# Kernel tuning notes

Hardware: AMD Instinct MI355X
Metric: run time of the kernel (lower is better)

Reference implementation:

```python
import jax, jax.numpy as jnp
import numpy as np

V, E = 50000, 800000
NODE_IN, EDGE_IN, OUT, HEADS = 128, 16, 32, 4
NEG_SLOPE = 0.2  # DGL EdgeGATConv default negative_slope


def setup_inputs() -> dict:
    key = jax.random.key(0)
    ks = jax.random.split(key, 10)
    return {
        "node_feats": jax.random.normal(ks[0], (V, NODE_IN), jnp.float32),
        "edge_feats": jax.random.normal(ks[1], (E, EDGE_IN), jnp.float32),
        "src": jax.random.randint(ks[2], (E,), 0, V),
        "dst": jax.random.randint(ks[3], (E,), 0, V),
        "W_node": jax.random.normal(ks[4], (NODE_IN, HEADS * OUT), jnp.float32) * 0.05,
        "W_edge": jax.random.normal(ks[5], (EDGE_IN, HEADS * OUT), jnp.float32) * 0.05,
        "attn_l": jax.random.normal(ks[6], (HEADS, OUT), jnp.float32) * 0.05,
        "attn_r": jax.random.normal(ks[7], (HEADS, OUT), jnp.float32) * 0.05,
        "attn_e": jax.random.normal(ks[8], (HEADS, OUT), jnp.float32) * 0.05,
        "res_W": jax.random.normal(ks[9], (NODE_IN, HEADS * OUT), jnp.float32) * 0.05,
        "bias": jnp.zeros((HEADS * OUT,), jnp.float32),
    }


def _leaky_relu(x, slope):
    return jnp.where(x >= 0, x, slope * x)


def reference(node_feats, edge_feats, src, dst, W_node, W_edge, attn_l, attn_r, attn_e, res_W, bias):
    V = node_feats.shape[0]
    H, F = attn_l.shape
    # linear projections
    ft = (node_feats @ W_node).reshape(V, H, F)    # [V,H,F]
    fe = (edge_feats @ W_edge).reshape(-1, H, F)   # [E,H,F]
    # per-head attention logits
    el = jnp.einsum('vhf,hf->vh', ft, attn_l)      # [V,H]
    er = jnp.einsum('vhf,hf->vh', ft, attn_r)      # [V,H]
    ee = jnp.einsum('ehf,hf->eh', fe, attn_e)      # [E,H]
    e = _leaky_relu(el[src] + er[dst] + ee, NEG_SLOPE)  # [E,H]
    # edge softmax over incoming edges of each destination node (stable)
    emax = jax.ops.segment_max(e, dst, num_segments=V)  # [V,H]
    ex = jnp.exp(e - emax[dst])
    esum = jax.ops.segment_sum(ex, dst, num_segments=V)  # [V,H]
    a = ex / esum[dst]                                   # [E,H]
    # weighted message passing: u_mul_e(ft, a) then sum to dst
    msg = ft[src] * a[:, :, None]                        # [E,H,F]
    rst = jax.ops.segment_sum(msg, dst, num_segments=V)  # [V,H,F]
    # residual connection + bias (EdgeGATConv residual=True, bias=True)
    rst = rst + (node_feats @ res_W).reshape(V, H, F)
    rst = rst + bias.reshape(1, H, F)
    # agg_mode='flatten': concat heads
    return rst.reshape(V, H * F)
```

## Files before the change

kernel.cpp:

```cpp
#include <hip/hip_runtime.h>
#include <hip/hip_fp16.h>
#include <cstdint>

#define V_N 50000
#define E_N 800000
#define NODE_IN 128
#define EDGE_IN 16
#define HF 128
#define NEG_SLOPE 0.2f
#define NB_SCAN 196

#define OFF_FT    0
#define OFF_EL    3200000
#define OFF_ER    3400000
#define OFF_DEG   3600000
#define OFF_ROW   3650000
#define OFF_BSUM  3700004
#define OFF_RANK  3700260
#define OFF_REC   4500260
#define OFF_WATT  7700260
#define OFF_BFRAG 7700324

typedef short bf16x8 __attribute__((ext_vector_type(8)));
typedef float f32x4 __attribute__((ext_vector_type(4)));

__device__ __forceinline__ unsigned short f2bf(float f) {
    unsigned u = __float_as_uint(f);
    u += 0x7fffu + ((u >> 16) & 1u);
    return (unsigned short)(u >> 16);
}
__device__ __forceinline__ unsigned pk2(float lo, float hi) {
    return (unsigned)f2bf(lo) | ((unsigned)f2bf(hi) << 16);
}
__device__ __forceinline__ float bflo(unsigned w) { return __uint_as_float(w << 16); }
__device__ __forceinline__ float bfhi(unsigned w) { return __uint_as_float(w & 0xffff0000u); }

typedef __fp16 fp16x2 __attribute__((ext_vector_type(2)));
__device__ __forceinline__ unsigned pkh2(float a, float b) {
    fp16x2 h = __builtin_amdgcn_cvt_pkrtz(a, b);
    return __builtin_bit_cast(unsigned, h);
}
__device__ __forceinline__ __half2 u2h(unsigned u) {
    return __builtin_bit_cast(__half2, u);
}
__device__ __forceinline__ unsigned h2u(__half2 h) {
    return __builtin_bit_cast(unsigned, h);
}

__global__ void k_prep(const float* __restrict__ We,
                       const float* __restrict__ attn_e,
                       const float* __restrict__ Wn,
                       const float* __restrict__ Wr,
                       float* __restrict__ watt,
                       unsigned* __restrict__ bfrag,
                       int* __restrict__ deg) {
    int g = blockIdx.x * 256 + threadIdx.x;
    for (int i = g; i < V_N; i += 16384) deg[i] = 0;
    if (blockIdx.x == 0 && threadIdx.x < 64) {
        int k = threadIdx.x >> 2, h = threadIdx.x & 3;
        float s = 0.f;
        #pragma unroll
        for (int f = 0; f < 32; f++)
            s += We[k * HF + h * 32 + f] * attn_e[h * 32 + f];
        watt[k * 4 + h] = s;
    }
    if (g < 16384) {
        int c    = g >> 8;
        int lane = (g >> 2) & 63;
        int jp   = g & 3;
        int nt = c >> 2, ks = c & 3;
        int col = nt * 16 + (lane & 15);
        int k   = ks * 32 + (lane >> 4) * 8 + jp * 2;
        const float* W = (col < 128) ? Wn : Wr;
        int cc = col & 127;
        float x0 = W[(size_t)k * 128 + cc];
        float x1 = W[(size_t)(k + 1) * 128 + cc];
        bfrag[g] = pk2(x0, x1);
    }
}

__global__ __launch_bounds__(256) void k_node(
    const float* __restrict__ nf, const unsigned* __restrict__ bfragw,
    const float* __restrict__ attn_l, const float* __restrict__ attn_r,
    const float* __restrict__ bias,
    unsigned* __restrict__ ftw, float* __restrict__ el,
    float* __restrict__ er, float* __restrict__ out)
{
    __shared__ __align__(16) float sSf[32 * 140];
    unsigned short* sA = (unsigned short*)sSf;

    const int t = threadIdx.x;
    const int lane = t & 63;
    const int w = t >> 6;
    const int nb = blockIdx.x * 32;
    const int n15 = lane & 15;
    const int q = lane >> 4;
    const unsigned short* bfrag = (const unsigned short*)bfragw;

    #pragma unroll
    for (int i = 0; i < 4; i++) {
        int f = t + i * 256;
        int node = f >> 5;
        int kc = (f & 31) * 4;
        float4 v = {0.f, 0.f, 0.f, 0.f};
        if (nb + node < V_N)
            v = *(const float4*)(nf + (size_t)(nb + node) * NODE_IN + kc);
        uint2 u2 = make_uint2(pk2(v.x, v.y), pk2(v.z, v.w));
        *(uint2*)&sA[node * 136 + kc] = u2;
    }
    __syncthreads();

    f32x4 acc[2][4];
    #pragma unroll
    for (int m = 0; m < 2; m++)
        #pragma unroll
        for (int tt = 0; tt < 4; tt++) acc[m][tt] = (f32x4){0.f, 0.f, 0.f, 0.f};

    #pragma unroll
    for (int ks = 0; ks < 4; ks++) {
        bf16x8 a0 = *(const bf16x8*)&sA[n15 * 136 + ks * 32 + q * 8];
        bf16x8 a1 = *(const bf16x8*)&sA[(16 + n15) * 136 + ks * 32 + q * 8];
        #pragma unroll
        for (int tt = 0; tt < 4; tt++) {
            int nt = (tt < 2) ? (2 * w + tt) : (8 + 2 * w + (tt - 2));
            bf16x8 b = *(const bf16x8*)(bfrag + ((size_t)(nt * 4 + ks) * 64 + lane) * 8);
            acc[0][tt] = __builtin_amdgcn_mfma_f32_16x16x32_bf16(a0, b, acc[0][tt], 0, 0, 0);
            acc[1][tt] = __builtin_amdgcn_mfma_f32_16x16x32_bf16(a1, b, acc[1][tt], 0, 0, 0);
        }
    }

    {
        float al0 = attn_l[w * 32 + n15];
        float al1 = attn_l[w * 32 + 16 + n15];
        float ar0 = attn_r[w * 32 + n15];
        float ar1 = attn_r[w * 32 + 16 + n15];
        #pragma unroll
        for (int m = 0; m < 2; m++) {
            #pragma unroll
            for (int r = 0; r < 4; r++) {
                float fa = acc[m][0][r], fb = acc[m][1][r];
                float elp = fa * al0 + fb * al1;
                float erp = fa * ar0 + fb * ar1;
                elp += __shfl_xor(elp, 1); erp += __shfl_xor(erp, 1);
                elp += __shfl_xor(elp, 2); erp += __shfl_xor(erp, 2);
                elp += __shfl_xor(elp, 4); erp += __shfl_xor(erp, 4);
                elp += __shfl_xor(elp, 8); erp += __shfl_xor(erp, 8);
                int node = nb + m * 16 + q * 4 + r;
                if (n15 == 0 && node < V_N) {
                    el[node * 4 + w] = elp;
                    er[node * 4 + w] = erp;
                }
            }
        }
    }
    #pragma unroll
    for (int m = 0; m < 2; m++)
        #pragma unroll
        for (int r = 0; r < 4; r++) {
            int node = nb + m * 16 + q * 4 + r;
            if (node < V_N)
                ftw[(size_t)node * 64 + w * 16 + n15] =
                    pkh2(acc[m][0][r], acc[m][1][r]);
        }
    __syncthreads();

    #pragma unroll
    for (int m = 0; m < 2; m++)
        #pragma unroll
        for (int tt = 2; tt < 4; tt++)
            #pragma unroll
            for (int r = 0; r < 4; r++)
                sSf[(m * 16 + q * 4 + r) * 140 + w * 32 + (tt - 2) * 16 + n15] =
                    acc[m][tt][r];
    __syncthreads();
    #pragma unroll
    for (int i = 0; i < 4; i++) {
        int u = t + i * 256;
        int node = u >> 5, c4 = (u & 31) * 4;
        if (nb + node < V_N) {
            float4 v = *(float4*)&sSf[node * 140 + c4];
            float4 b4 = *(const float4*)(bias + c4);
            v.x += b4.x; v.y += b4.y; v.z += b4.z; v.w += b4.w;
            *(float4*)(out + (size_t)(nb + node) * HF + c4) = v;
        }
    }
}

__global__ void k_hist(const int* __restrict__ dst, int* __restrict__ deg,
                       int* __restrict__ rank) {
    int e = blockIdx.x * 256 + threadIdx.x;
    if (e < E_N) rank[e] = atomicAdd(&deg[dst[e]], 1);
}

__global__ __launch_bounds__(256) void k_scan1(const int* __restrict__ deg,
                                               int* __restrict__ rowp,
                                               int* __restrict__ bsum) {
    __shared__ int sh[256];
    int t = threadIdx.x, b = blockIdx.x;
    int i = b * 256 + t;
    int v = (i < V_N) ? deg[i] : 0;
    sh[t] = v;
    __syncthreads();
    #pragma unroll
    for (int off = 1; off < 256; off <<= 1) {
        int u = (t >= off) ? sh[t - off] : 0;
        __syncthreads();
        sh[t] += u;
        __syncthreads();
    }
    if (i < V_N) rowp[i] = sh[t] - v;
    if (t == 255) bsum[b] = sh[255];
}

__global__ __launch_bounds__(256) void k_scan23(int* __restrict__ rowp,
                                                const int* __restrict__ bsum) {
    __shared__ int sh[256];
    int t = threadIdx.x, b = blockIdx.x;
    int v = (t < NB_SCAN) ? bsum[t] : 0;
    sh[t] = v;
    __syncthreads();
    #pragma unroll
    for (int off = 1; off < 256; off <<= 1) {
        int u = (t >= off) ? sh[t - off] : 0;
        __syncthreads();
        sh[t] += u;
        __syncthreads();
    }
    int boff = (b == 0) ? 0 : sh[b - 1];
    int i = b * 256 + t;
    if (i < V_N) rowp[i] += boff;
    if (i == 0) rowp[V_N] = E_N;
}

__global__ __launch_bounds__(256) void k_escatter(
    const float* __restrict__ ef, const int* __restrict__ src,
    const int* __restrict__ dst, const int* __restrict__ rank,
    const int* __restrict__ rowp, const float* __restrict__ watt,
    const float* __restrict__ el, uint4* __restrict__ rec)
{
    __shared__ float sw[64];
    __shared__ __align__(16) float see[256][4];
    const int t = threadIdx.x;
    if (t < 64) sw[t] = watt[t];
    __syncthreads();
    const int base = blockIdx.x * 256;
    const int lane = t & 63, w = t >> 6;
    const int k0 = (lane & 3) * 4;

    #pragma unroll
    for (int r = 0; r < 4; r++) {
        int le = w * 64 + r * 16 + (lane >> 2);
        float4 v = *(const float4*)(ef + (size_t)(base + le) * EDGE_IN + k0);
        float e0 = 0.f, e1 = 0.f, e2 = 0.f, e3 = 0.f;
        float vv[4] = {v.x, v.y, v.z, v.w};
        #pragma unroll
        for (int j = 0; j < 4; j++) {
            int k = k0 + j;
            e0 += vv[j] * sw[k * 4 + 0];
            e1 += vv[j] * sw[k * 4 + 1];
            e2 += vv[j] * sw[k * 4 + 2];
            e3 += vv[j] * sw[k * 4 + 3];
        }
        e0 += __shfl_xor(e0, 1); e1 += __shfl_xor(e1, 1);
        e2 += __shfl_xor(e2, 1); e3 += __shfl_xor(e3, 1);
        e0 += __shfl_xor(e0, 2); e1 += __shfl_xor(e1, 2);
        e2 += __shfl_xor(e2, 2); e3 += __shfl_xor(e3, 2);
        if ((lane & 3) == 0) {
            float4 o = {e0, e1, e2, e3};
            *(float4*)&see[le][0] = o;
        }
    }
    __syncthreads();

    int e = base + t;
    int s = src[e], d = dst[e];
    int p = rowp[d] + rank[e];
    float4 ee = *(float4*)&see[t][0];
    float4 el4 = *(const float4*)(el + (size_t)s * 4);
    uint4 rr;
    rr.x = (unsigned)s;
    rr.y = pk2(el4.x + ee.x, el4.y + ee.y);
    rr.z = pk2(el4.z + ee.z, el4.w + ee.w);
    rr.w = 0;
    rec[p] = rr;
}

__global__ __launch_bounds__(256) void k_gather(
    const int* __restrict__ row, const uint4* __restrict__ rec,
    const float* __restrict__ er,
    const unsigned* __restrict__ ftw, float* __restrict__ out)
{
    __shared__ unsigned aw[4][64][4];
    const int lane = threadIdx.x & 63;
    const int wid  = threadIdx.x >> 6;
    const int d = blockIdx.x * 4 + wid;
    if (d >= V_N) return;
    const int n0 = row[d];
    const int deg = row[d + 1] - n0;
    if (deg == 0) return;

    const float4 er4 = *(const float4*)(er + (size_t)d * 4);

    const int qw = lane >> 4, li = lane & 15;
    const int head = li >> 2;
    float4 s4 = {0.f, 0.f, 0.f, 0.f};
    __half2 ha0 = u2h(0u), ha1 = u2h(0u), ha2 = u2h(0u), ha3 = u2h(0u);
    __half2 hb0 = u2h(0u), hb1 = u2h(0u), hb2 = u2h(0u), hb3 = u2h(0u);

    for (int i0 = 0; i0 < deg; i0 += 64) {
        int chunk = min(64, deg - i0);
        int si = 0;
        float4 ex = {0.f, 0.f, 0.f, 0.f};
        if (lane < chunk) {
            uint4 r = rec[n0 + i0 + lane];
            si = (int)r.x;
            float x0 = bflo(r.y) + er4.x;
            float x1 = bfhi(r.y) + er4.y;
            float x2 = bflo(r.z) + er4.z;
            float x3 = bfhi(r.z) + er4.w;
            x0 = x0 >= 0.f ? x0 : NEG_SLOPE * x0;
            x1 = x1 >= 0.f ? x1 : NEG_SLOPE * x1;
            x2 = x2 >= 0.f ? x2 : NEG_SLOPE * x2;
            x3 = x3 >= 0.f ? x3 : NEG_SLOPE * x3;
            ex.x = __expf(x0); ex.y = __expf(x1);
            ex.z = __expf(x2); ex.w = __expf(x3);
            s4.x += ex.x; s4.y += ex.y; s4.z += ex.z; s4.w += ex.w;
        }
        uint4 ap;
        ap.x = pkh2(ex.x, ex.x); ap.y = pkh2(ex.y, ex.y);
        ap.z = pkh2(ex.z, ex.z); ap.w = pkh2(ex.w, ex.w);
        *(uint4*)&aw[wid][lane][0] = ap;
        asm volatile("s_waitcnt lgkmcnt(0)" ::: "memory");

        int iters = (chunk + 7) & ~7;
        for (int j = 0; j < iters; j += 8) {
            int jq0 = j + qw, jq1 = j + qw + 4;
            int sidx0 = __shfl(si, jq0);
            int sidx1 = __shfl(si, jq1);
            unsigned au0 = aw[wid][jq0][head];
            unsigned au1 = aw[wid][jq1][head];
            uint4 wv0 = *(const uint4*)(ftw + (size_t)sidx0 * 64 + li * 4);
            uint4 wv1 = *(const uint4*)(ftw + (size_t)sidx1 * 64 + li * 4);
            ha0 = __hfma2(u2h(wv0.x), u2h(au0), ha0);
            ha1 = __hfma2(u2h(wv0.y), u2h(au0), ha1);
            ha2 = __hfma2(u2h(wv0.z), u2h(au0), ha2);
            ha3 = __hfma2(u2h(wv0.w), u2h(au0), ha3);
            hb0 = __hfma2(u2h(wv1.x), u2h(au1), hb0);
            hb1 = __hfma2(u2h(wv1.y), u2h(au1), hb1);
            hb2 = __hfma2(u2h(wv1.z), u2h(au1), hb2);
            hb3 = __hfma2(u2h(wv1.w), u2h(au1), hb3);
        }
    }
    #pragma unroll
    for (int off = 1; off < 64; off <<= 1) {
        s4.x += __shfl_xor(s4.x, off);
        s4.y += __shfl_xor(s4.y, off);
        s4.z += __shfl_xor(s4.z, off);
        s4.w += __shfl_xor(s4.w, off);
    }
    ha0 = __hadd2(ha0, hb0); ha1 = __hadd2(ha1, hb1);
    ha2 = __hadd2(ha2, hb2); ha3 = __hadd2(ha3, hb3);
    ha0 = __hadd2(ha0, u2h(__shfl_xor(h2u(ha0), 16)));
    ha1 = __hadd2(ha1, u2h(__shfl_xor(h2u(ha1), 16)));
    ha2 = __hadd2(ha2, u2h(__shfl_xor(h2u(ha2), 16)));
    ha3 = __hadd2(ha3, u2h(__shfl_xor(h2u(ha3), 16)));
    ha0 = __hadd2(ha0, u2h(__shfl_xor(h2u(ha0), 32)));
    ha1 = __hadd2(ha1, u2h(__shfl_xor(h2u(ha1), 32)));
    ha2 = __hadd2(ha2, u2h(__shfl_xor(h2u(ha2), 32)));
    ha3 = __hadd2(ha3, u2h(__shfl_xor(h2u(ha3), 32)));
    if (qw == 0) {
        float rsv = 1.f / (head == 0 ? s4.x : head == 1 ? s4.y :
                           head == 2 ? s4.z : s4.w);
        float* op = out + (size_t)d * HF + head * 32 + (li & 3) * 4;
        float4 r0 = *(float4*)op;
        r0.x += __low2float(ha0) * rsv; r0.y += __low2float(ha1) * rsv;
        r0.z += __low2float(ha2) * rsv; r0.w += __low2float(ha3) * rsv;
        *(float4*)op = r0;
        float4 r1 = *(float4*)(op + 16);
        r1.x += __high2float(ha0) * rsv; r1.y += __high2float(ha1) * rsv;
        r1.z += __high2float(ha2) * rsv; r1.w += __high2float(ha3) * rsv;
        *(float4*)(op + 16) = r1;
    }
}

extern "C" void kernel_launch(void* const* d_in, const int* in_sizes, int n_in,
                              void* d_out, int out_size, void* d_ws, size_t ws_size,
                              hipStream_t stream) {
    const float* nf     = (const float*)d_in[0];
    const float* ef     = (const float*)d_in[1];
    const int*   src    = (const int*)d_in[2];
    const int*   dst    = (const int*)d_in[3];
    const float* Wn     = (const float*)d_in[4];
    const float* We     = (const float*)d_in[5];
    const float* attn_l = (const float*)d_in[6];
    const float* attn_r = (const float*)d_in[7];
    const float* attn_e = (const float*)d_in[8];
    const float* Wr     = (const float*)d_in[9];
    const float* bias   = (const float*)d_in[10];
    float* out = (float*)d_out;

    unsigned* wsw  = (unsigned*)d_ws;
    unsigned* ftw  = wsw + OFF_FT;
    float* el      = (float*)(wsw + OFF_EL);
    float* er      = (float*)(wsw + OFF_ER);
    int* deg       = (int*)(wsw + OFF_DEG);
    int* rowp      = (int*)(wsw + OFF_ROW);
    int* bsum      = (int*)(wsw + OFF_BSUM);
    int* rank      = (int*)(wsw + OFF_RANK);
    uint4* rec     = (uint4*)(wsw + OFF_REC);
    float* watt    = (float*)(wsw + OFF_WATT);
    unsigned* bfrag = wsw + OFF_BFRAG;

    k_prep<<<64, 256, 0, stream>>>(We, attn_e, Wn, Wr, watt, bfrag, deg);
    k_hist<<<(E_N + 255) / 256, 256, 0, stream>>>(dst, deg, rank);
    k_scan1<<<NB_SCAN, 256, 0, stream>>>(deg, rowp, bsum);
    k_scan23<<<NB_SCAN, 256, 0, stream>>>(rowp, bsum);
    k_node<<<(V_N + 31) / 32, 256, 0, stream>>>(nf, bfrag, attn_l, attn_r,
                                                bias, ftw, el, er, out);
    k_escatter<<<E_N / 256, 256, 0, stream>>>(ef, src, dst, rank,
                                              rowp, watt, el, rec);
    k_gather<<<(V_N + 3) / 4, 256, 0, stream>>>(rowp, rec, er, ftw, out);
}
```

Baseline: 243.1 us.

## Fuse prep, histogram, node GEMM and scan into one cooperative kernel

Merges the five setup kernels (weight prep, degree histogram, node projection GEMM, two-level scan) into a single cooperative kernel of 512 persistent blocks, with grid.sync between the dependent phases. The histogram and the node GEMM now run in the same phase and can overlap. The aim is to remove several kernel launch gaps and tail effects. In exchange it adds grid-wide barriers, uses a smaller grid for the GEMM and histogram work, and requires all 512 blocks to be co-resident.

```diff
diff --git a/kernel.cpp b/kernel.cpp
--- a/kernel.cpp
+++ b/kernel.cpp
@@ -1,6 +1,9 @@
 #include <hip/hip_runtime.h>
 #include <hip/hip_fp16.h>
+#include <hip/hip_cooperative_groups.h>
 #include <cstdint>
+
+namespace cg = cooperative_groups;
 
 #define V_N 50000
 #define E_N 800000
@@ -9,6 +12,7 @@
 #define HF 128
 #define NEG_SLOPE 0.2f
 #define NB_SCAN 196
+#define COOP_GRID 512
 
 #define OFF_FT    0
 #define OFF_EL    3200000
@@ -47,17 +51,33 @@
     return __builtin_bit_cast(unsigned, h);
 }
 
-__global__ void k_prep(const float* __restrict__ We,
-                       const float* __restrict__ attn_e,
-                       const float* __restrict__ Wn,
-                       const float* __restrict__ Wr,
-                       float* __restrict__ watt,
-                       unsigned* __restrict__ bfrag,
-                       int* __restrict__ deg) {
-    int g = blockIdx.x * 256 + threadIdx.x;
-    for (int i = g; i < V_N; i += 16384) deg[i] = 0;
-    if (blockIdx.x == 0 && threadIdx.x < 64) {
-        int k = threadIdx.x >> 2, h = threadIdx.x & 3;
+__global__ __launch_bounds__(256, 2) void k_setup(
+    const float* __restrict__ nf,
+    const float* __restrict__ We, const float* __restrict__ attn_e,
+    const float* __restrict__ Wn, const float* __restrict__ Wr,
+    const float* __restrict__ attn_l, const float* __restrict__ attn_r,
+    const float* __restrict__ bias,
+    const int* __restrict__ dst,
+    float* __restrict__ watt, unsigned* __restrict__ bfragw,
+    int* __restrict__ deg, int* __restrict__ rank,
+    int* __restrict__ rowp, int* __restrict__ bsum,
+    unsigned* __restrict__ ftw, float* __restrict__ el,
+    float* __restrict__ er, float* __restrict__ out)
+{
+    cg::grid_group grid = cg::this_grid();
+
+    __shared__ __align__(16) float sSf[32 * 140];
+    unsigned short* sA = (unsigned short*)sSf;
+    int* sh = (int*)sSf;
+
+    const int t = threadIdx.x;
+    const int b = blockIdx.x;
+    const int g = b * 256 + t;
+    const int GSZ = COOP_GRID * 256;
+
+    if (g < V_N) deg[g] = 0;
+    if (b == 0 && t < 64) {
+        int k = t >> 2, h = t & 3;
         float s = 0.f;
         #pragma unroll
         for (int f = 0; f < 32; f++)
@@ -75,161 +95,146 @@
         int cc = col & 127;
         float x0 = W[(size_t)k * 128 + cc];
         float x1 = W[(size_t)(k + 1) * 128 + cc];
-        bfrag[g] = pk2(x0, x1);
-    }
-}
-
-__global__ __launch_bounds__(256) void k_node(
-    const float* __restrict__ nf, const unsigned* __restrict__ bfragw,
-    const float* __restrict__ attn_l, const float* __restrict__ attn_r,
-    const float* __restrict__ bias,
-    unsigned* __restrict__ ftw, float* __restrict__ el,
-    float* __restrict__ er, float* __restrict__ out)
-{
-    __shared__ __align__(16) float sSf[32 * 140];
-    unsigned short* sA = (unsigned short*)sSf;
-
-    const int t = threadIdx.x;
-    const int lane = t & 63;
-    const int w = t >> 6;
-    const int nb = blockIdx.x * 32;
-    const int n15 = lane & 15;
-    const int q = lane >> 4;
-    const unsigned short* bfrag = (const unsigned short*)bfragw;
-
-    #pragma unroll
-    for (int i = 0; i < 4; i++) {
-        int f = t + i * 256;
-        int node = f >> 5;
-        int kc = (f & 31) * 4;
-        float4 v = {0.f, 0.f, 0.f, 0.f};
-        if (nb + node < V_N)
-            v = *(const float4*)(nf + (size_t)(nb + node) * NODE_IN + kc);
-        uint2 u2 = make_uint2(pk2(v.x, v.y), pk2(v.z, v.w));
-        *(uint2*)&sA[node * 136 + kc] = u2;
-    }
-    __syncthreads();
-
-    f32x4 acc[2][4];
-    #pragma unroll
-    for (int m = 0; m < 2; m++)
-        #pragma unroll
-        for (int tt = 0; tt < 4; tt++) acc[m][tt] = (f32x4){0.f, 0.f, 0.f, 0.f};
-
-    #pragma unroll
-    for (int ks = 0; ks < 4; ks++) {
-        bf16x8 a0 = *(const bf16x8*)&sA[n15 * 136 + ks * 32 + q * 8];
-        bf16x8 a1 = *(const bf16x8*)&sA[(16 + n15) * 136 + ks * 32 + q * 8];
-        #pragma unroll
-        for (int tt = 0; tt < 4; tt++) {
-            int nt = (tt < 2) ? (2 * w + tt) : (8 + 2 * w + (tt - 2));
-            bf16x8 b = *(const bf16x8*)(bfrag + ((size_t)(nt * 4 + ks) * 64 + lane) * 8);
-            acc[0][tt] = __builtin_amdgcn_mfma_f32_16x16x32_bf16(a0, b, acc[0][tt], 0, 0, 0);
-            acc[1][tt] = __builtin_amdgcn_mfma_f32_16x16x32_bf16(a1, b, acc[1][tt], 0, 0, 0);
-        }
-    }
+        bfragw[g] = pk2(x0, x1);
+    }
+    grid.sync();
+
+    for (int e = g; e < E_N; e += GSZ)
+        rank[e] = atomicAdd(&deg[dst[e]], 1);
 
     {
-        float al0 = attn_l[w * 32 + n15];
-        float al1 = attn_l[w * 32 + 16 + n15];
-        float ar0 = attn_r[w * 32 + n15];
-        float ar1 = attn_r[w * 32 + 16 + n15];
-        #pragma unroll
-        for (int m = 0; m < 2; m++) {
-            #pragma unroll
-            for (int r = 0; r < 4; r++) {
-                float fa = acc[m][0][r], fb = acc[m][1][r];
-                float elp = fa * al0 + fb * al1;
-                float erp = fa * ar0 + fb * ar1;
-                elp += __shfl_xor(elp, 1); erp += __shfl_xor(erp, 1);
-                elp += __shfl_xor(elp, 2); erp += __shfl_xor(erp, 2);
-                elp += __shfl_xor(elp, 4); erp += __shfl_xor(erp, 4);
-                elp += __shfl_xor(elp, 8); erp += __shfl_xor(erp, 8);
-                int node = nb + m * 16 + q * 4 + r;
-                if (n15 == 0 && node < V_N) {
-                    el[node * 4 + w] = elp;
-                    er[node * 4 + w] = erp;
+        const int lane = t & 63;
+        const int w = t >> 6;
+        const int n15 = lane & 15;
+        const int q = lane >> 4;
+        const unsigned short* bfrag = (const unsigned short*)bfragw;
+        const float al0 = attn_l[w * 32 + n15];
+        const float al1 = attn_l[w * 32 + 16 + n15];
+        const float ar0 = attn_r[w * 32 + n15];
+        const float ar1 = attn_r[w * 32 + 16 + n15];
+
+        for (int tile = b; tile < (V_N + 31) / 32; tile += COOP_GRID) {
+            const int nb = tile * 32;
+            __syncthreads();
+
+            #pragma unroll
+            for (int i = 0; i < 4; i++) {
+                int f = t + i * 256;
+                int node = f >> 5;
+                int kc = (f & 31) * 4;
+                float4 v = {0.f, 0.f, 0.f, 0.f};
+                if (nb + node < V_N)
+                    v = *(const float4*)(nf + (size_t)(nb + node) * NODE_IN + kc);
+                uint2 u2 = make_uint2(pk2(v.x, v.y), pk2(v.z, v.w));
+                *(uint2*)&sA[node * 136 + kc] = u2;
+            }
+            __syncthreads();
+
+            f32x4 acc[2][4];
+            #pragma unroll
+            for (int m = 0; m < 2; m++)
+                #pragma unroll
+                for (int tt = 0; tt < 4; tt++) acc[m][tt] = (f32x4){0.f, 0.f, 0.f, 0.f};
+
+            #pragma unroll
+            for (int ks = 0; ks < 4; ks++) {
+                bf16x8 a0 = *(const bf16x8*)&sA[n15 * 136 + ks * 32 + q * 8];
+                bf16x8 a1 = *(const bf16x8*)&sA[(16 + n15) * 136 + ks * 32 + q * 8];
+                #pragma unroll
+                for (int tt = 0; tt < 4; tt++) {
+                    int nt = (tt < 2) ? (2 * w + tt) : (8 + 2 * w + (tt - 2));
+                    bf16x8 bv = *(const bf16x8*)(bfrag + ((size_t)(nt * 4 + ks) * 64 + lane) * 8);
+                    acc[0][tt] = __builtin_amdgcn_mfma_f32_16x16x32_bf16(a0, bv, acc[0][tt], 0, 0, 0);
+                    acc[1][tt] = __builtin_amdgcn_mfma_f32_16x16x32_bf16(a1, bv, acc[1][tt], 0, 0, 0);
                 }
             }
-        }
-    }
-    #pragma unroll
-    for (int m = 0; m < 2; m++)
+
+            #pragma unroll
+            for (int m = 0; m < 2; m++) {
+                #pragma unroll
+                for (int r = 0; r < 4; r++) {
+                    float fa = acc[m][0][r], fb = acc[m][1][r];
+                    float elp = fa * al0 + fb * al1;
+                    float erp = fa * ar0 + fb * ar1;
+                    elp += __shfl_xor(elp, 1); erp += __shfl_xor(erp, 1);
+                    elp += __shfl_xor(elp, 2); erp += __shfl_xor(erp, 2);
+                    elp += __shfl_xor(elp, 4); erp += __shfl_xor(erp, 4);
+                    elp += __shfl_xor(elp, 8); erp += __shfl_xor(erp, 8);
+                    int node = nb + m * 16 + q * 4 + r;
+                    if (n15 == 0 && node < V_N) {
+                        el[node * 4 + w] = elp;
+                        er[node * 4 + w] = erp;
+                    }
+                }
+            }
+            #pragma unroll
+            for (int m = 0; m < 2; m++)
+                #pragma unroll
+                for (int r = 0; r < 4; r++) {
+                    int node = nb + m * 16 + q * 4 + r;
+                    if (node < V_N)
+                        ftw[(size_t)node * 64 + w * 16 + n15] =
+                            pkh2(acc[m][0][r], acc[m][1][r]);
+                }
+            __syncthreads();
+
+            #pragma unroll
+            for (int m = 0; m < 2; m++)
+                #pragma unroll
+                for (int tt = 2; tt < 4; tt++)
+                    #pragma unroll
+                    for (int r = 0; r < 4; r++)
+                        sSf[(m * 16 + q * 4 + r) * 140 + w * 32 + (tt - 2) * 16 + n15] =
+                            acc[m][tt][r];
+            __syncthreads();
+            #pragma unroll
+            for (int i = 0; i < 4; i++) {
+                int u = t + i * 256;
+                int node = u >> 5, c4 = (u & 31) * 4;
+                if (nb + node < V_N) {
+                    float4 v = *(float4*)&sSf[node * 140 + c4];
+                    float4 b4 = *(const float4*)(bias + c4);
+                    v.x += b4.x; v.y += b4.y; v.z += b4.z; v.w += b4.w;
+                    *(float4*)(out + (size_t)(nb + node) * HF + c4) = v;
+                }
+            }
+        }
+    }
+    grid.sync();
+
+    if (b < NB_SCAN) {
+        int i = b * 256 + t;
+        int v = (i < V_N) ? deg[i] : 0;
+        sh[t] = v;
+        __syncthreads();
         #pragma unroll
-        for (int r = 0; r < 4; r++) {
-            int node = nb + m * 16 + q * 4 + r;
-            if (node < V_N)
-                ftw[(size_t)node * 64 + w * 16 + n15] =
-                    pkh2(acc[m][0][r], acc[m][1][r]);
-        }
-    __syncthreads();
-
-    #pragma unroll
-    for (int m = 0; m < 2; m++)
+        for (int off = 1; off < 256; off <<= 1) {
+            int u = (t >= off) ? sh[t - off] : 0;
+            __syncthreads();
+            sh[t] += u;
+            __syncthreads();
+        }
+        if (i < V_N) rowp[i] = sh[t] - v;
+        if (t == 255) bsum[b] = sh[255];
+    }
+    grid.sync();
+
+    if (b < NB_SCAN) {
+        int v = (t < NB_SCAN) ? bsum[t] : 0;
+        sh[t] = v;
+        __syncthreads();
         #pragma unroll
-        for (int tt = 2; tt < 4; tt++)
-            #pragma unroll
-            for (int r = 0; r < 4; r++)
-                sSf[(m * 16 + q * 4 + r) * 140 + w * 32 + (tt - 2) * 16 + n15] =
-                    acc[m][tt][r];
-    __syncthreads();
-    #pragma unroll
-    for (int i = 0; i < 4; i++) {
-        int u = t + i * 256;
-        int node = u >> 5, c4 = (u & 31) * 4;
-        if (nb + node < V_N) {
-            float4 v = *(float4*)&sSf[node * 140 + c4];
-            float4 b4 = *(const float4*)(bias + c4);
-            v.x += b4.x; v.y += b4.y; v.z += b4.z; v.w += b4.w;
-            *(float4*)(out + (size_t)(nb + node) * HF + c4) = v;
-        }
-    }
-}
-
-__global__ void k_hist(const int* __restrict__ dst, int* __restrict__ deg,
-                       int* __restrict__ rank) {
-    int e = blockIdx.x * 256 + threadIdx.x;
-    if (e < E_N) rank[e] = atomicAdd(&deg[dst[e]], 1);
-}
-
-__global__ __launch_bounds__(256) void k_scan1(const int* __restrict__ deg,
-                                               int* __restrict__ rowp,
-                                               int* __restrict__ bsum) {
-    __shared__ int sh[256];
-    int t = threadIdx.x, b = blockIdx.x;
-    int i = b * 256 + t;
-    int v = (i < V_N) ? deg[i] : 0;
-    sh[t] = v;
-    __syncthreads();
-    #pragma unroll
-    for (int off = 1; off < 256; off <<= 1) {
-        int u = (t >= off) ? sh[t - off] : 0;
-        __syncthreads();
-        sh[t] += u;
-        __syncthreads();
-    }
-    if (i < V_N) rowp[i] = sh[t] - v;
-    if (t == 255) bsum[b] = sh[255];
-}
-
-__global__ __launch_bounds__(256) void k_scan23(int* __restrict__ rowp,
-                                                const int* __restrict__ bsum) {
-    __shared__ int sh[256];
-    int t = threadIdx.x, b = blockIdx.x;
-    int v = (t < NB_SCAN) ? bsum[t] : 0;
-    sh[t] = v;
-    __syncthreads();
-    #pragma unroll
-    for (int off = 1; off < 256; off <<= 1) {
-        int u = (t >= off) ? sh[t - off] : 0;
-        __syncthreads();
-        sh[t] += u;
-        __syncthreads();
-    }
-    int boff = (b == 0) ? 0 : sh[b - 1];
-    int i = b * 256 + t;
-    if (i < V_N) rowp[i] += boff;
-    if (i == 0) rowp[V_N] = E_N;
+        for (int off = 1; off < 256; off <<= 1) {
+            int u = (t >= off) ? sh[t - off] : 0;
+            __syncthreads();
+            sh[t] += u;
+            __syncthreads();
+        }
+        int boff = (b == 0) ? 0 : sh[b - 1];
+        int i = b * 256 + t;
+        if (i < V_N) rowp[i] += boff;
+        if (i == 0) rowp[V_N] = E_N;
+    }
 }
 
 __global__ __launch_bounds__(256) void k_escatter(
@@ -411,12 +416,15 @@
     float* watt    = (float*)(wsw + OFF_WATT);
     unsigned* bfrag = wsw + OFF_BFRAG;
 
-    k_prep<<<64, 256, 0, stream>>>(We, attn_e, Wn, Wr, watt, bfrag, deg);
-    k_hist<<<(E_N + 255) / 256, 256, 0, stream>>>(dst, deg, rank);
-    k_scan1<<<NB_SCAN, 256, 0, stream>>>(deg, rowp, bsum);
-    k_scan23<<<NB_SCAN, 256, 0, stream>>>(rowp, bsum);
-    k_node<<<(V_N + 31) / 32, 256, 0, stream>>>(nf, bfrag, attn_l, attn_r,
-                                                bias, ftw, el, er, out);
+    void* args[] = {
+        (void*)&nf, (void*)&We, (void*)&attn_e, (void*)&Wn, (void*)&Wr,
+        (void*)&attn_l, (void*)&attn_r, (void*)&bias, (void*)&dst,
+        (void*)&watt, (void*)&bfrag, (void*)&deg, (void*)&rank,
+        (void*)&rowp, (void*)&bsum, (void*)&ftw, (void*)&el, (void*)&er,
+        (void*)&out
+    };
+    hipLaunchCooperativeKernel((void*)k_setup, dim3(COOP_GRID), dim3(256),
+                               args, 0, stream);
     k_escatter<<<E_N / 256, 256, 0, stream>>>(ef, src, dst, rank,
                                               rowp, watt, el, rec);
     k_gather<<<(V_N + 3) / 4, 256, 0, stream>>>(rowp, rec, er, ftw, out);
```

Measured after the change: 421.9 us. 1.74x slower.

## Fuse degree histogram into node GEMM kernel and collapse scan into one pass

Applied to the files above, without the earlier changes.

The edge-degree histogram kernel is merged into the node projection kernel as extra trailing blocks, so both independent workloads share one launch and can overlap. The two-stage block scan is replaced by a single kernel in which each block recomputes its prefix by summing all preceding degrees directly. Together these remove two kernel launches and the idle gaps between them. In exchange, later scan blocks do redundant reads that grow with block index (up to about 50K ints each), and the fused kernel carries GEMM shared-memory allocation even for histogram blocks.

```diff
diff --git a/kernel.cpp b/kernel.cpp
--- a/kernel.cpp
+++ b/kernel.cpp
@@ -9,6 +9,8 @@
 #define HF 128
 #define NEG_SLOPE 0.2f
 #define NB_SCAN 196
+#define NODE_BLKS 1563
+#define HIST_BLKS 3125
 
 #define OFF_FT    0
 #define OFF_EL    3200000
@@ -79,15 +81,22 @@
     }
 }
 
-__global__ __launch_bounds__(256) void k_node(
+__global__ __launch_bounds__(256) void k_nodehist(
     const float* __restrict__ nf, const unsigned* __restrict__ bfragw,
     const float* __restrict__ attn_l, const float* __restrict__ attn_r,
-    const float* __restrict__ bias,
+    const float* __restrict__ bias, const int* __restrict__ dst,
     unsigned* __restrict__ ftw, float* __restrict__ el,
-    float* __restrict__ er, float* __restrict__ out)
+    float* __restrict__ er, float* __restrict__ out,
+    int* __restrict__ deg, int* __restrict__ rank)
 {
     __shared__ __align__(16) float sSf[32 * 140];
     unsigned short* sA = (unsigned short*)sSf;
+
+    if (blockIdx.x >= NODE_BLKS) {
+        int e = (blockIdx.x - NODE_BLKS) * 256 + threadIdx.x;
+        rank[e] = atomicAdd(&deg[dst[e]], 1);
+        return;
+    }
 
     const int t = threadIdx.x;
     const int lane = t & 63;
@@ -186,17 +195,23 @@
     }
 }
 
-__global__ void k_hist(const int* __restrict__ dst, int* __restrict__ deg,
-                       int* __restrict__ rank) {
-    int e = blockIdx.x * 256 + threadIdx.x;
-    if (e < E_N) rank[e] = atomicAdd(&deg[dst[e]], 1);
-}
-
-__global__ __launch_bounds__(256) void k_scan1(const int* __restrict__ deg,
-                                               int* __restrict__ rowp,
-                                               int* __restrict__ bsum) {
+__global__ __launch_bounds__(256) void k_scan(const int* __restrict__ deg,
+                                              int* __restrict__ rowp) {
     __shared__ int sh[256];
     int t = threadIdx.x, b = blockIdx.x;
+
+    int pre = 0;
+    for (int i = t; i < b * 256; i += 256) pre += deg[i];
+    sh[t] = pre;
+    __syncthreads();
+    #pragma unroll
+    for (int off = 128; off > 0; off >>= 1) {
+        if (t < off) sh[t] += sh[t + off];
+        __syncthreads();
+    }
+    int sbase = sh[0];
+    __syncthreads();
+
     int i = b * 256 + t;
     int v = (i < V_N) ? deg[i] : 0;
     sh[t] = v;
@@ -208,27 +223,7 @@
         sh[t] += u;
         __syncthreads();
     }
-    if (i < V_N) rowp[i] = sh[t] - v;
-    if (t == 255) bsum[b] = sh[255];
-}
-
-__global__ __launch_bounds__(256) void k_scan23(int* __restrict__ rowp,
-                                                const int* __restrict__ bsum) {
-    __shared__ int sh[256];
-    int t = threadIdx.x, b = blockIdx.x;
-    int v = (t < NB_SCAN) ? bsum[t] : 0;
-    sh[t] = v;
-    __syncthreads();
-    #pragma unroll
-    for (int off = 1; off < 256; off <<= 1) {
-        int u = (t >= off) ? sh[t - off] : 0;
-        __syncthreads();
-        sh[t] += u;
-        __syncthreads();
-    }
-    int boff = (b == 0) ? 0 : sh[b - 1];
-    int i = b * 256 + t;
-    if (i < V_N) rowp[i] += boff;
+    if (i < V_N) rowp[i] = sbase + sh[t] - v;
     if (i == 0) rowp[V_N] = E_N;
 }
 
@@ -405,18 +400,15 @@
     float* er      = (float*)(wsw + OFF_ER);
     int* deg       = (int*)(wsw + OFF_DEG);
     int* rowp      = (int*)(wsw + OFF_ROW);
-    int* bsum      = (int*)(wsw + OFF_BSUM);
     int* rank      = (int*)(wsw + OFF_RANK);
     uint4* rec     = (uint4*)(wsw + OFF_REC);
     float* watt    = (float*)(wsw + OFF_WATT);
     unsigned* bfrag = wsw + OFF_BFRAG;
 
     k_prep<<<64, 256, 0, stream>>>(We, attn_e, Wn, Wr, watt, bfrag, deg);
-    k_hist<<<(E_N + 255) / 256, 256, 0, stream>>>(dst, deg, rank);
-    k_scan1<<<NB_SCAN, 256, 0, stream>>>(deg, rowp, bsum);
-    k_scan23<<<NB_SCAN, 256, 0, stream>>>(rowp, bsum);
-    k_node<<<(V_N + 31) / 32, 256, 0, stream>>>(nf, bfrag, attn_l, attn_r,
-                                                bias, ftw, el, er, out);
+    k_nodehist<<<NODE_BLKS + HIST_BLKS, 256, 0, stream>>>(
+        nf, bfrag, attn_l, attn_r, bias, dst, ftw, el, er, out, deg, rank);
+    k_scan<<<NB_SCAN, 256, 0, stream>>>(deg, rowp);
     k_escatter<<<E_N / 256, 256, 0, stream>>>(ef, src, dst, rank,
                                               rowp, watt, el, rec);
     k_gather<<<(V_N + 3) / 4, 256, 0, stream>>>(rowp, rec, er, ftw, out);
```

Measured after the change: 256.8 us. +5.6%, slower.
